# Kernel optimization log

Measured on AMD Instinct MI355X. Metric: run time of the kernel, lower is better.

## Reference

```python
import jax, jax.numpy as jnp
import numpy as np

N, E, G = 150000, 300000, 4096   # nodes, edges, graphs
H, L = 256, 7                    # hidden_channels, num_gc_layers
ATOM_FEATS, ATOM_VOCAB = 9, 64
BOND_FEATS, BOND_VOCAB = 3, 8
BN_EPS = 1e-5
MSG_EPS = 1e-7


def setup_inputs() -> dict:
    key = jax.random.key(0)
    ks = jax.random.split(key, 10)
    return dict(
        x=jax.random.randint(ks[0], (N, ATOM_FEATS), 0, ATOM_VOCAB),
        edge_index=jax.random.randint(ks[1], (2, E), 0, N),
        edge_attr=jax.random.randint(ks[2], (E, BOND_FEATS), 0, BOND_VOCAB),
        batch=jnp.sort(jax.random.randint(ks[3], (N,), 0, G)),
        atom_emb=jax.random.normal(ks[4], (ATOM_FEATS, ATOM_VOCAB, H), jnp.float32) * 0.02,
        bond_emb=jax.random.normal(ks[5], (BOND_FEATS, BOND_VOCAB, H), jnp.float32) * 0.02,
        vn_weight=jnp.zeros((1, H), jnp.float32),  # Embedding(1,H) init to 0
        conv_w=jax.random.normal(ks[6], (L, H, H), jnp.float32) / np.float32(np.sqrt(H)),
        conv_b=jnp.zeros((L, H), jnp.float32),
        norm_gamma=jnp.ones((L, H), jnp.float32),
        norm_beta=jnp.zeros((L, H), jnp.float32),
        vn_w=jax.random.normal(ks[7], (L - 1, 2, H, H), jnp.float32) / np.float32(np.sqrt(H)),
        vn_b=jnp.zeros((L - 1, 2, H), jnp.float32),
        vn_gamma=jnp.ones((L - 1, 2, H), jnp.float32),
        vn_beta=jnp.zeros((L - 1, 2, H), jnp.float32),
    )


def _bn(x, gamma, beta):
    # BatchNorm1d in training mode (biased batch stats over the node axis)
    mu = jnp.mean(x, axis=0)
    var = jnp.mean(jnp.square(x - mu), axis=0)
    return (x - mu) * jax.lax.rsqrt(var + BN_EPS) * gamma + beta


def _genconv(h, src, dst, edge_emb, w, b):
    # GENConv, aggr='add', mlp_layers=1: msg = relu(x_j + e) + eps; out = Linear(x + sum_agg)
    msg = jax.nn.relu(h[src] + edge_emb) + MSG_EPS            # [E,H]
    agg = jax.ops.segment_sum(msg, dst, num_segments=N)       # [N,H]
    return (h + agg) @ w + b


def reference(x, edge_index, edge_attr, batch, atom_emb, bond_emb, vn_weight,
              conv_w, conv_b, norm_gamma, norm_beta, vn_w, vn_b, vn_gamma, vn_beta):
    src, dst = edge_index[0], edge_index[1]
    # AtomEncoder: sum of per-feature embeddings
    h = jnp.take(atom_emb[0], x[:, 0], axis=0)
    for f in range(1, ATOM_FEATS):
        h = h + jnp.take(atom_emb[f], x[:, f], axis=0)
    # virtual node embedding (one per graph, gathered init from Embedding(1,H))
    vn = jnp.broadcast_to(vn_weight[0], (G, H))
    h = h + vn[batch]
    # BondEncoder (conv_encode_edge=False -> encode once)
    edge_emb = jnp.take(bond_emb[0], edge_attr[:, 0], axis=0)
    for f in range(1, BOND_FEATS):
        edge_emb = edge_emb + jnp.take(bond_emb[f], edge_attr[:, f], axis=0)
    # res+ block: GENConv -> [BN -> ReLU -> VN update -> GENConv -> +res]*
    h = _genconv(h, src, dst, edge_emb, conv_w[0], conv_b[0])
    for layer in range(1, L):
        h2 = jax.nn.relu(_bn(h, norm_gamma[layer - 1], norm_beta[layer - 1]))
        # virtual node: pool + residual, 2-layer MLP (Linear->BN->ReLU twice)
        vn_t = jax.ops.segment_sum(h2, batch, num_segments=G) + vn
        for j in range(2):
            vn_t = jax.nn.relu(_bn(vn_t @ vn_w[layer - 1, j] + vn_b[layer - 1, j],
                                   vn_gamma[layer - 1, j], vn_beta[layer - 1, j]))
        vn = vn_t
        h2 = h2 + vn[batch]
        h = _genconv(h2, src, dst, edge_emb, conv_w[layer], conv_b[layer]) + h
    h = _bn(h, norm_gamma[L - 1], norm_beta[L - 1])
    return jax.ops.segment_sum(h, batch, num_segments=G)  # global_add_pool -> [G,H]
```

## Files before the change

### kernel.cpp

```cpp
#include <hip/hip_runtime.h>
#include <hip/hip_bf16.h>


#define Ncnt 150000
#define Ecnt 300000
#define Gcnt 4096
#define Hc 256
#define Lcnt 7
#define BN_EPS 1e-5f
#define MSG_EPS 1e-7f

typedef __hip_bfloat16 bf16;
typedef __attribute__((ext_vector_type(8))) short bf16x8;
typedef __attribute__((ext_vector_type(8))) unsigned short u16x8;
typedef __attribute__((ext_vector_type(4))) float f32x4;

static __device__ __forceinline__ int imin(int a, int b) { return a < b ? a : b; }

static __device__ __forceinline__ float bs2f(unsigned short s) {
  unsigned u = ((unsigned)s) << 16;
  union { unsigned u; float f; } c; c.u = u; return c.f;
}
static __device__ __forceinline__ unsigned short f2bs(float f) {
  bf16 h = __float2bfloat16(f);
  union { bf16 h; unsigned short s; } c; c.h = h; return c.s;
}
static __device__ __forceinline__ float4 bf4tof4(ushort4 u) {
  float4 r; r.x = bs2f(u.x); r.y = bs2f(u.y); r.z = bs2f(u.z); r.w = bs2f(u.w); return r;
}
static __device__ __forceinline__ ushort4 f4tobf4(float4 v) {
  ushort4 u; u.x = f2bs(v.x); u.y = f2bs(v.y); u.z = f2bs(v.z); u.w = f2bs(v.w); return u;
}

static __device__ __forceinline__ void gll16(const bf16* g, const short* l) {
  __builtin_amdgcn_global_load_lds((const __attribute__((address_space(1))) void*)g,
                                   (__attribute__((address_space(3))) void*)l, 16, 0, 0);
}

__global__ __launch_bounds__(256) void k_zero(float* __restrict__ p, int n) {
  int i = blockIdx.x * 256 + threadIdx.x;
  if (i < n) p[i] = 0.f;
}
__global__ __launch_bounds__(256) void k_zero_int(int* __restrict__ p, int n) {
  int i = blockIdx.x * 256 + threadIdx.x;
  if (i < n) p[i] = 0;
}
__global__ void k_diag(float* __restrict__ out, float v) { out[0] = v; }

__global__ __launch_bounds__(256) void k_bnprep(float* __restrict__ stats,
                                                const float* __restrict__ gamma, const float* __restrict__ beta,
                                                float* __restrict__ scb, float* __restrict__ bbb, float invM) {
  int c = threadIdx.x;
  float mu = stats[c] * invM;
  float var = stats[Hc + c] * invM - mu * mu;
  float sc = rsqrtf(var + BN_EPS) * gamma[c];
  scb[c] = sc;
  bbb[c] = beta[c] - mu * sc;
  stats[c] = 0.f;
  stats[Hc + c] = 0.f;
}

__global__ __launch_bounds__(256) void k_count(const int* __restrict__ ei, int* __restrict__ cnt) {
  int e = blockIdx.x * 256 + threadIdx.x;
  if (e < Ecnt) atomicAdd(&cnt[ei[Ecnt + e]], 1);
}
__global__ __launch_bounds__(256) void k_scan1(const int* __restrict__ cnt, int* __restrict__ rowptr,
                                               int* __restrict__ bsum, int n) {
  __shared__ int sh[256];
  int t = threadIdx.x;
  int i = blockIdx.x * 256 + t;
  int v = (i < n) ? cnt[i] : 0;
  sh[t] = v;
  __syncthreads();
#pragma unroll
  for (int off = 1; off < 256; off <<= 1) {
    int u = (t >= off) ? sh[t - off] : 0;
    __syncthreads();
    sh[t] += u;
    __syncthreads();
  }
  if (i < n) rowptr[i] = sh[t] - v;
  if (t == 255) bsum[blockIdx.x] = sh[255];
}
__global__ __launch_bounds__(1024) void k_scan2(int* __restrict__ bsum, int nb) {
  __shared__ int sh[1024];
  int t = threadIdx.x;
  int v = (t < nb) ? bsum[t] : 0;
  sh[t] = v;
  __syncthreads();
#pragma unroll
  for (int off = 1; off < 1024; off <<= 1) {
    int u = (t >= off) ? sh[t - off] : 0;
    __syncthreads();
    sh[t] += u;
    __syncthreads();
  }
  if (t < nb) bsum[t] = sh[t] - v;
}
__global__ __launch_bounds__(256) void k_scan3(int* __restrict__ rowptr, int* __restrict__ cursor,
                                               const int* __restrict__ bsum, int n) {
  int i = blockIdx.x * 256 + threadIdx.x;
  if (i < n) {
    int v = rowptr[i] + bsum[blockIdx.x];
    rowptr[i] = v;
    cursor[i] = v;
  }
  if (i == 0) rowptr[n] = Ecnt;
}
__global__ __launch_bounds__(256) void k_scatter(const int* __restrict__ ei, const int* __restrict__ ea,
                                                 const int* __restrict__ batch, int* __restrict__ cursor,
                                                 int2* __restrict__ erec) {
  int e = blockIdx.x * 256 + threadIdx.x;
  if (e < Ecnt) {
    int d = ei[Ecnt + e];
    int s = ei[e];
    int packed = ea[e * 3] | (ea[e * 3 + 1] << 3) | (ea[e * 3 + 2] << 6) | (batch[s] << 9);
    int pos = atomicAdd(&cursor[d], 1);
    erec[pos] = make_int2(s, packed);
  }
}

__global__ __launch_bounds__(256) void k_prep_w(const float* __restrict__ W, bf16* __restrict__ hi,
                                                bf16* __restrict__ lo, int nmats) {
  int c = blockIdx.x * 256 + threadIdx.x;
  if (c >= nmats * 8192) return;
  int lane = c & 63;
  int t = c >> 6;
  int kc8 = t & 7;
  int nt = (t >> 3) & 15;
  int m = t >> 7;
  int n = nt * 16 + (lane & 15);
  int k0 = kc8 * 32 + (lane >> 4) * 8;
  bf16x8 hv, lv;
#pragma unroll
  for (int j = 0; j < 8; ++j) {
    float w = W[(size_t)m * 65536 + (size_t)(k0 + j) * 256 + n];
    unsigned short h = f2bs(w);
    float res = w - bs2f(h);
    hv[j] = (short)h;
    lv[j] = (short)f2bs(res);
  }
  *(bf16x8*)&hi[(size_t)c * 8] = hv;
  *(bf16x8*)&lo[(size_t)c * 8] = lv;
}

__global__ __launch_bounds__(256) void k_atom_encode(const int* __restrict__ x,
                                                     const float* __restrict__ aemb,
                                                     const float* __restrict__ vnw,
                                                     bf16* __restrict__ P) {
  int wave = threadIdx.x >> 6, lane = threadIdx.x & 63;
  int r = blockIdx.x * 4 + wave;
  if (r >= Ncnt) return;
  int c4 = lane * 4;
  const int* xr = x + (size_t)r * 9;
  float4 v = *(const float4*)&vnw[c4];
#pragma unroll
  for (int f = 0; f < 9; ++f) {
    float4 e = *(const float4*)&aemb[(size_t)((f << 6) + xr[f]) * Hc + c4];
    v.x += e.x; v.y += e.y; v.z += e.z; v.w += e.w;
  }
  *(ushort4*)&P[(size_t)r * Hc + c4] = f4tobf4(v);
}

__global__ __launch_bounds__(256) void k_init_vn(float* __restrict__ vn, float* __restrict__ vnt,
                                                 const float* __restrict__ vnw) {
  int idx = blockIdx.x * 256 + threadIdx.x;
  float v = vnw[idx & (Hc - 1)];
  vn[idx] = v;
  vnt[idx] = v;
}

__global__ __launch_bounds__(256) void k_agg(const bf16* __restrict__ P, bf16* __restrict__ T,
                                             const int* __restrict__ rowptr, const int2* __restrict__ erec,
                                             const float* __restrict__ bemb,
                                             const float* __restrict__ vn, const int* __restrict__ batch,
                                             const float* __restrict__ scb, const float* __restrict__ bbb) {
  int hw = threadIdx.x >> 5, lane = threadIdx.x & 31;
  int r = blockIdx.x * 8 + hw;
  if (r >= Ncnt) return;
  int c8 = lane * 8;
  bool hasbn = (scb != nullptr);
  float sc[8], bb[8];
  if (hasbn) {
    float4 s0 = *(const float4*)&scb[c8], s1 = *(const float4*)&scb[c8 + 4];
    float4 b0 = *(const float4*)&bbb[c8], b1 = *(const float4*)&bbb[c8 + 4];
    sc[0] = s0.x; sc[1] = s0.y; sc[2] = s0.z; sc[3] = s0.w;
    sc[4] = s1.x; sc[5] = s1.y; sc[6] = s1.z; sc[7] = s1.w;
    bb[0] = b0.x; bb[1] = b0.y; bb[2] = b0.z; bb[3] = b0.w;
    bb[4] = b1.x; bb[5] = b1.y; bb[6] = b1.z; bb[7] = b1.w;
  }
  float acc[8];
  {
    u16x8 pv = *(const u16x8*)&P[(size_t)r * Hc + c8];
    if (hasbn) {
      const float* vr = &vn[(size_t)batch[r] * Hc + c8];
      float4 w0 = *(const float4*)vr, w1 = *(const float4*)(vr + 4);
      float w[8] = {w0.x, w0.y, w0.z, w0.w, w1.x, w1.y, w1.z, w1.w};
#pragma unroll
      for (int k = 0; k < 8; ++k) acc[k] = fmaxf(fmaf(bs2f(pv[k]), sc[k], bb[k]), 0.f) + w[k];
    } else {
#pragma unroll
      for (int k = 0; k < 8; ++k) acc[k] = bs2f(pv[k]);
    }
  }
  int j0 = rowptr[r], j1 = rowptr[r + 1];
  if (j0 < j1) {
    int2 er = erec[j0];
    for (int j = j0; j < j1; ++j) {
      int2 ern = (j + 1 < j1) ? erec[j + 1] : er;
      int s = er.x;
      int a0 = er.y & 7, a1 = (er.y >> 3) & 7, a2 = (er.y >> 6) & 7, g = er.y >> 9;
      u16x8 sv = *(const u16x8*)&P[(size_t)s * Hc + c8];
      const float* e0 = &bemb[(size_t)a0 * Hc + c8];
      const float* e1 = &bemb[(size_t)(8 + a1) * Hc + c8];
      const float* e2 = &bemb[(size_t)(16 + a2) * Hc + c8];
      float4 e0a = *(const float4*)e0, e0b = *(const float4*)(e0 + 4);
      float4 e1a = *(const float4*)e1, e1b = *(const float4*)(e1 + 4);
      float4 e2a = *(const float4*)e2, e2b = *(const float4*)(e2 + 4);
      float em[8] = {e0a.x + e1a.x + e2a.x, e0a.y + e1a.y + e2a.y,
                     e0a.z + e1a.z + e2a.z, e0a.w + e1a.w + e2a.w,
                     e0b.x + e1b.x + e2b.x, e0b.y + e1b.y + e2b.y,
                     e0b.z + e1b.z + e2b.z, e0b.w + e1b.w + e2b.w};
      if (hasbn) {
        const float* vr = &vn[(size_t)g * Hc + c8];
        float4 w0 = *(const float4*)vr, w1 = *(const float4*)(vr + 4);
        float w[8] = {w0.x, w0.y, w0.z, w0.w, w1.x, w1.y, w1.z, w1.w};
#pragma unroll
        for (int k = 0; k < 8; ++k) {
          float v = fmaxf(fmaf(bs2f(sv[k]), sc[k], bb[k]), 0.f) + w[k];
          acc[k] += fmaxf(v + em[k], 0.f) + MSG_EPS;
        }
      } else {
#pragma unroll
        for (int k = 0; k < 8; ++k)
          acc[k] += fmaxf(bs2f(sv[k]) + em[k], 0.f) + MSG_EPS;
      }
      er = ern;
    }
  }
  u16x8 ov;
#pragma unroll
  for (int k = 0; k < 8; ++k) ov[k] = f2bs(acc[k]);
  *(u16x8*)&T[(size_t)r * Hc + c8] = ov;
}

__global__ __launch_bounds__(256) void k_seg_vn(const bf16* __restrict__ P, const int* __restrict__ batch,
                                                float* __restrict__ vnt,
                                                const float* __restrict__ scb, const float* __restrict__ bbb) {
  int wave = threadIdx.x >> 6, lane = threadIdx.x & 63;
  int base = (blockIdx.x * 4 + wave) * 64;
  if (base >= Ncnt) return;
  int c4 = lane * 4;
  float4 scv = *(const float4*)&scb[c4];
  float4 bbv = *(const float4*)&bbb[c4];
  int end = imin(base + 64, Ncnt);
  float4 acc = make_float4(0.f, 0.f, 0.f, 0.f);
  int curg = batch[base];
  for (int r = base; r < end; ++r) {
    int g = batch[r];
    float4 v = bf4tof4(*(const ushort4*)&P[(size_t)r * Hc + c4]);
    v.x = fmaxf(fmaf(v.x, scv.x, bbv.x), 0.f); v.y = fmaxf(fmaf(v.y, scv.y, bbv.y), 0.f);
    v.z = fmaxf(fmaf(v.z, scv.z, bbv.z), 0.f); v.w = fmaxf(fmaf(v.w, scv.w, bbv.w), 0.f);
    if (g != curg) {
      float* d = &vnt[(size_t)curg * Hc + c4];
      atomicAdd(d, acc.x); atomicAdd(d + 1, acc.y); atomicAdd(d + 2, acc.z); atomicAdd(d + 3, acc.w);
      acc = make_float4(0.f, 0.f, 0.f, 0.f);
      curg = g;
    }
    acc.x += v.x; acc.y += v.y; acc.z += v.z; acc.w += v.w;
  }
  float* d = &vnt[(size_t)curg * Hc + c4];
  atomicAdd(d, acc.x); atomicAdd(d + 1, acc.y); atomicAdd(d + 2, acc.z); atomicAdd(d + 3, acc.w);
}

__global__ __launch_bounds__(256) void k_vn_relu(const float* __restrict__ in, float* __restrict__ out,
                                                 float* __restrict__ out2,
                                                 const float* __restrict__ stats,
                                                 const float* __restrict__ gamma, const float* __restrict__ beta,
                                                 float invM) {
  int idx = blockIdx.x * 256 + threadIdx.x;
  int c = idx & (Hc - 1);
  float mu = stats[c] * invM;
  float var = stats[Hc + c] * invM - mu * mu;
  float sc = rsqrtf(var + BN_EPS) * gamma[c];
  float bb = beta[c] - mu * sc;
  float v = fmaxf(fmaf(in[idx], sc, bb), 0.f);
  out[idx] = v;
  out2[idx] = v;
}

__global__ __launch_bounds__(256) void k_bn_pool(const bf16* __restrict__ P, const int* __restrict__ batch,
                                                 float* __restrict__ out,
                                                 const float* __restrict__ scb, const float* __restrict__ bbb) {
  int wave = threadIdx.x >> 6, lane = threadIdx.x & 63;
  int base = (blockIdx.x * 4 + wave) * 64;
  if (base >= Ncnt) return;
  int c4 = lane * 4;
  float4 scv = *(const float4*)&scb[c4];
  float4 bbv = *(const float4*)&bbb[c4];
  int end = imin(base + 64, Ncnt);
  float4 acc = make_float4(0.f, 0.f, 0.f, 0.f);
  int curg = batch[base];
  for (int r = base; r < end; ++r) {
    int g = batch[r];
    float4 v = bf4tof4(*(const ushort4*)&P[(size_t)r * Hc + c4]);
    v.x = fmaf(v.x, scv.x, bbv.x); v.y = fmaf(v.y, scv.y, bbv.y);
    v.z = fmaf(v.z, scv.z, bbv.z); v.w = fmaf(v.w, scv.w, bbv.w);
    if (g != curg) {
      float* d = &out[(size_t)curg * Hc + c4];
      atomicAdd(d, acc.x); atomicAdd(d + 1, acc.y); atomicAdd(d + 2, acc.z); atomicAdd(d + 3, acc.w);
      acc = make_float4(0.f, 0.f, 0.f, 0.f);
      curg = g;
    }
    acc.x += v.x; acc.y += v.y; acc.z += v.z; acc.w += v.w;
  }
  float* d = &out[(size_t)curg * Hc + c4];
  atomicAdd(d, acc.x); atomicAdd(d + 1, acc.y); atomicAdd(d + 2, acc.z); atomicAdd(d + 3, acc.w);
}

__global__ __launch_bounds__(256, 3) void k_gemm_mfma(const bf16* __restrict__ A, const bf16* __restrict__ Whi,
                                                      const bf16* __restrict__ Wlo, const float* __restrict__ bias,
                                                      const bf16* __restrict__ R, bf16* __restrict__ C,
                                                      float* __restrict__ stats, int M) {
  __shared__ __attribute__((aligned(16))) short As[64 * 64];
  __shared__ __attribute__((aligned(16))) unsigned short Cs[16 * 264];
  __shared__ float lsum[256], lsq[256];
  int tid = threadIdx.x;
  int wave = tid >> 6, lane = tid & 63;
  int quad = lane >> 4, l15 = lane & 15;
  int wc = wave * 64;
  int row0 = blockIdx.x * 64;

  lsum[tid] = 0.f;
  lsq[tid] = 0.f;

  int sr[2], sjg[2];
#pragma unroll
  for (int i = 0; i < 2; ++i) {
    int s = i * 256 + tid;
    sr[i] = s >> 3;
    sjg[i] = (s & 7) ^ (sr[i] & 7);
  }

  f32x4 acc[4][4];
#pragma unroll
  for (int i = 0; i < 4; ++i)
#pragma unroll
    for (int j = 0; j < 4; ++j) acc[i][j] = (f32x4){0.f, 0.f, 0.f, 0.f};

  for (int kci = 0; kci < 4; ++kci) {
    int kc = kci * 64;
#pragma unroll
    for (int i = 0; i < 2; ++i) {
      int ar = row0 + sr[i]; if (ar >= M) ar = M - 1;
      gll16(A + (size_t)ar * Hc + kc + sjg[i] * 8, &As[(i * 256 + wave * 64) * 8]);
    }
    __syncthreads();
#pragma unroll
    for (int ks = 0; ks < 2; ++ks) {
      int kc8 = kci * 2 + ks;
      int g = ks * 4 + quad;
      bf16x8 af[4];
#pragma unroll
      for (int mi = 0; mi < 4; ++mi) {
        int row = mi * 16 + l15;
        af[mi] = *(const bf16x8*)&As[row * 64 + (g ^ (row & 7)) * 8];
      }
#pragma unroll
      for (int nii = 0; nii < 4; ++nii) {
        int nt = wave * 4 + nii;
        size_t fo = (((size_t)nt * 8 + kc8) * 64 + lane) * 8;
        bf16x8 bh = *(const bf16x8*)&Whi[fo];
        bf16x8 bl = *(const bf16x8*)&Wlo[fo];
#pragma unroll
        for (int mi = 0; mi < 4; ++mi) {
          acc[mi][nii] = __builtin_amdgcn_mfma_f32_16x16x32_bf16(af[mi], bh, acc[mi][nii], 0, 0, 0);
          acc[mi][nii] = __builtin_amdgcn_mfma_f32_16x16x32_bf16(af[mi], bl, acc[mi][nii], 0, 0, 0);
        }
      }
    }
    __syncthreads();
  }

  float s8[8], q8[8];
#pragma unroll
  for (int k = 0; k < 8; ++k) { s8[k] = 0.f; q8[k] = 0.f; }
  int cg8 = (tid & 31) * 8;

  for (int p = 0; p < 4; ++p) {
    int lr0 = quad * 4;
#pragma unroll
    for (int ni = 0; ni < 4; ++ni) {
      int col = wc + ni * 16 + l15;
      float bcol = bias[col];
#pragma unroll
      for (int j = 0; j < 4; ++j)
        Cs[(lr0 + j) * 264 + col] = f2bs(acc[p][ni][j] + bcol);
    }
    __syncthreads();
#pragma unroll
    for (int i = 0; i < 2; ++i) {
      int slot = i * 256 + tid;
      int lr = slot >> 5;
      int grow = row0 + p * 16 + lr;
      if (grow < M) {
        u16x8 cv = *(const u16x8*)&Cs[lr * 264 + cg8];
        float v[8];
#pragma unroll
        for (int k = 0; k < 8; ++k) v[k] = bs2f(cv[k]);
        if (R) {
          u16x8 rv = *(const u16x8*)&R[(size_t)grow * Hc + cg8];
#pragma unroll
          for (int k = 0; k < 8; ++k) v[k] += bs2f(rv[k]);
        }
        u16x8 ov;
#pragma unroll
        for (int k = 0; k < 8; ++k) {
          ov[k] = f2bs(v[k]);
          s8[k] += v[k];
          q8[k] = fmaf(v[k], v[k], q8[k]);
        }
        *(u16x8*)&C[(size_t)grow * Hc + cg8] = ov;
      }
    }
    __syncthreads();
  }

#pragma unroll
  for (int k = 0; k < 8; ++k) {
    atomicAdd(&lsum[cg8 + k], s8[k]);
    atomicAdd(&lsq[cg8 + k], q8[k]);
  }
  __syncthreads();
  atomicAdd(&stats[tid], lsum[tid]);
  atomicAdd(&stats[Hc + tid], lsq[tid]);
}

__global__ __launch_bounds__(256) void k_gemm_f32(const float* __restrict__ A, const float* __restrict__ W,
                                                  const float* __restrict__ bias, float* __restrict__ C,
                                                  float* __restrict__ statsOut,
                                                  const float* __restrict__ statsIn,
                                                  const float* __restrict__ gIn, const float* __restrict__ bIn,
                                                  float invM, int M) {
  __shared__ float As[64][68];
  __shared__ float Ws[64][68];
  __shared__ float lsum[64], lsq[64];
  int tid = threadIdx.x;
  int row0 = blockIdx.x * 64;
  int col0 = blockIdx.y * 64;
  int tx = tid & 15, ty = tid >> 4;
  if (tid < 64) { lsum[tid] = 0.f; lsq[tid] = 0.f; }
  float acc[4][4] = {{0.f}};
  for (int k0 = 0; k0 < 256; k0 += 64) {
#pragma unroll
    for (int i = 0; i < 4; ++i) {
      int lin = tid + i * 256;
      int r = lin >> 4;
      int c4 = (lin & 15) << 2;
      int gr = row0 + r;
      float4 v = make_float4(0.f, 0.f, 0.f, 0.f);
      if (gr < M) v = *(const float4*)&A[(size_t)gr * Hc + k0 + c4];
      if (statsIn) {
        float4 sv = *(const float4*)&statsIn[k0 + c4];
        float4 qv = *(const float4*)&statsIn[Hc + k0 + c4];
        float4 gv = *(const float4*)&gIn[k0 + c4];
        float4 bv = *(const float4*)&bIn[k0 + c4];
        float mu, var, sc, bb;
        mu = sv.x * invM; var = qv.x * invM - mu * mu; sc = rsqrtf(var + BN_EPS) * gv.x; bb = bv.x - mu * sc;
        v.x = fmaxf(fmaf(v.x, sc, bb), 0.f);
        mu = sv.y * invM; var = qv.y * invM - mu * mu; sc = rsqrtf(var + BN_EPS) * gv.y; bb = bv.y - mu * sc;
        v.y = fmaxf(fmaf(v.y, sc, bb), 0.f);
        mu = sv.z * invM; var = qv.z * invM - mu * mu; sc = rsqrtf(var + BN_EPS) * gv.z; bb = bv.z - mu * sc;
        v.z = fmaxf(fmaf(v.z, sc, bb), 0.f);
        mu = sv.w * invM; var = qv.w * invM - mu * mu; sc = rsqrtf(var + BN_EPS) * gv.w; bb = bv.w - mu * sc;
        v.w = fmaxf(fmaf(v.w, sc, bb), 0.f);
      }
      As[r][c4] = v.x; As[r][c4 + 1] = v.y; As[r][c4 + 2] = v.z; As[r][c4 + 3] = v.w;
      float4 w = *(const float4*)&W[(size_t)(k0 + r) * Hc + col0 + c4];
      Ws[r][c4] = w.x; Ws[r][c4 + 1] = w.y; Ws[r][c4 + 2] = w.z; Ws[r][c4 + 3] = w.w;
    }
    __syncthreads();
#pragma unroll
    for (int k = 0; k < 64; ++k) {
      float a[4], w[4];
#pragma unroll
      for (int i = 0; i < 4; ++i) a[i] = As[ty * 4 + i][k];
#pragma unroll
      for (int j = 0; j < 4; ++j) w[j] = Ws[k][tx * 4 + j];
#pragma unroll
      for (int i = 0; i < 4; ++i)
#pragma unroll
        for (int j = 0; j < 4; ++j) acc[i][j] = fmaf(a[i], w[j], acc[i][j]);
    }
    __syncthreads();
  }
  float cs[4] = {0.f, 0.f, 0.f, 0.f}, cq[4] = {0.f, 0.f, 0.f, 0.f};
#pragma unroll
  for (int i = 0; i < 4; ++i) {
    int gr = row0 + ty * 4 + i;
    if (gr >= M) break;
#pragma unroll
    for (int j = 0; j < 4; ++j) {
      int gc = col0 + tx * 4 + j;
      float v = acc[i][j] + bias[gc];
      C[(size_t)gr * Hc + gc] = v;
      cs[j] += v;
      cq[j] = fmaf(v, v, cq[j]);
    }
  }
#pragma unroll
  for (int j = 0; j < 4; ++j) {
    atomicAdd(&lsum[tx * 4 + j], cs[j]);
    atomicAdd(&lsq[tx * 4 + j], cq[j]);
  }
  __syncthreads();
  if (tid < 64) {
    atomicAdd(&statsOut[col0 + tid], lsum[tid]);
    atomicAdd(&statsOut[Hc + col0 + tid], lsq[tid]);
  }
}

extern "C" void kernel_launch(void* const* d_in, const int* in_sizes, int n_in,
                              void* d_out, int out_size, void* d_ws, size_t ws_size,
                              hipStream_t stream) {
  const int* x = (const int*)d_in[0];
  const int* ei = (const int*)d_in[1];
  const int* ea = (const int*)d_in[2];
  const int* batch = (const int*)d_in[3];
  const float* aemb = (const float*)d_in[4];
  const float* bemb = (const float*)d_in[5];
  const float* vnw = (const float*)d_in[6];
  const float* conv_w = (const float*)d_in[7];
  const float* conv_b = (const float*)d_in[8];
  const float* ngamma = (const float*)d_in[9];
  const float* nbeta = (const float*)d_in[10];
  const float* vn_w = (const float*)d_in[11];
  const float* vn_b = (const float*)d_in[12];
  const float* vn_g = (const float*)d_in[13];
  const float* vn_be = (const float*)d_in[14];
  float* out = (float*)d_out;

  const size_t NODE = (size_t)Ncnt * Hc;
  const size_t GH = (size_t)Gcnt * Hc;
  const int nScanBlk = (Ncnt + 255) / 256;

  size_t off = 0;
  char* base = (char*)d_ws;
  auto take = [&](size_t bytes) { size_t o = off; off += (bytes + 15) & ~(size_t)15; return o; };
  float* vn = (float*)(base + take(GH * 4));
  float* vnt = (float*)(base + take(GH * 4));
  float* vnu = (float*)(base + take(GH * 4));
  float* vnv = (float*)(base + take(GH * 4));
  float* statsN = (float*)(base + take(2 * Hc * 4));
  float* statsV1 = (float*)(base + take(2 * Hc * 4));
  float* statsV2 = (float*)(base + take(2 * Hc * 4));
  float* scbN = (float*)(base + take(Hc * 4));
  float* bbbN = (float*)(base + take(Hc * 4));
  int* rowptr = (int*)(base + take((size_t)(Ncnt + 1) * 4));
  int* cursor = (int*)(base + take((size_t)Ncnt * 4));
  int2* erec = (int2*)(base + take((size_t)Ecnt * 8));
  int* bsum = (int*)(base + take((size_t)nScanBlk * 4));
  bf16* P = (bf16*)(base + take(NODE * 2));
  bf16* T = (bf16*)(base + take(NODE * 2));
  bf16* WhiC = (bf16*)(base + take((size_t)Lcnt * 65536 * 2));
  bf16* WloC = (bf16*)(base + take((size_t)Lcnt * 65536 * 2));
  const size_t NEED = off;
  if (ws_size < NEED) {
    k_zero<<<(int)((GH + 255) / 256), 256, 0, stream>>>(out, (int)GH);
    k_diag<<<1, 1, 0, stream>>>(out, 100000.f + (float)(ws_size / (1024.0 * 1024.0)));
    return;
  }

  const int eBlk = (Ecnt + 255) / 256;
  const int nWaveBlk = (Ncnt + 3) / 4;
  const int aggBlk = (Ncnt + 7) / 8;
  const int segBlk = (Ncnt + 255) / 256;
  const int ggN = (Ncnt + 63) / 64;
  const dim3 gv(Gcnt / 64, 4);
  const float invN = 1.f / Ncnt;
  const float invG = 1.f / Gcnt;

  k_zero_int<<<nScanBlk, 256, 0, stream>>>(cursor, Ncnt);
  k_count<<<eBlk, 256, 0, stream>>>(ei, cursor);
  k_scan1<<<nScanBlk, 256, 0, stream>>>(cursor, rowptr, bsum, Ncnt);
  k_scan2<<<1, 1024, 0, stream>>>(bsum, nScanBlk);
  k_scan3<<<nScanBlk, 256, 0, stream>>>(rowptr, cursor, bsum, Ncnt);
  k_scatter<<<eBlk, 256, 0, stream>>>(ei, ea, batch, cursor, erec);

  k_prep_w<<<(Lcnt * 8192 + 255) / 256, 256, 0, stream>>>(conv_w, WhiC, WloC, Lcnt);

  k_atom_encode<<<nWaveBlk, 256, 0, stream>>>(x, aemb, vnw, P);
  k_init_vn<<<(int)(GH / 256), 256, 0, stream>>>(vn, vnt, vnw);
  k_agg<<<aggBlk, 256, 0, stream>>>(P, T, rowptr, erec, bemb, nullptr, nullptr, nullptr, nullptr);
  k_zero<<<2, 256, 0, stream>>>(statsN, 2 * Hc);
  k_gemm_mfma<<<ggN, 256, 0, stream>>>(T, WhiC, WloC, conv_b, nullptr, P, statsN, Ncnt);

  for (int l = 1; l < Lcnt; ++l) {
    int p = l - 1;
    k_bnprep<<<1, 256, 0, stream>>>(statsN, ngamma + (size_t)p * Hc, nbeta + (size_t)p * Hc,
                                    scbN, bbbN, invN);
    k_seg_vn<<<segBlk, 256, 0, stream>>>(P, batch, vnt, scbN, bbbN);
    k_zero<<<4, 256, 0, stream>>>(statsV1, 4 * Hc);
    k_gemm_f32<<<gv, 256, 0, stream>>>(vnt, vn_w + (size_t)(2 * p) * 65536,
                                       vn_b + (size_t)(2 * p) * Hc, vnu, statsV1,
                                       nullptr, nullptr, nullptr, invG, Gcnt);
    k_gemm_f32<<<gv, 256, 0, stream>>>(vnu, vn_w + (size_t)(2 * p + 1) * 65536,
                                       vn_b + (size_t)(2 * p + 1) * Hc, vnv, statsV2,
                                       statsV1, vn_g + (size_t)(2 * p) * Hc,
                                       vn_be + (size_t)(2 * p) * Hc, invG, Gcnt);
    k_vn_relu<<<(int)(GH / 256), 256, 0, stream>>>(vnv, vn, vnt, statsV2,
                                                   vn_g + (size_t)(2 * p + 1) * Hc,
                                                   vn_be + (size_t)(2 * p + 1) * Hc, invG);
    k_agg<<<aggBlk, 256, 0, stream>>>(P, T, rowptr, erec, bemb, vn, batch, scbN, bbbN);
    k_gemm_mfma<<<ggN, 256, 0, stream>>>(T, WhiC + (size_t)l * 65536, WloC + (size_t)l * 65536,
                                         conv_b + (size_t)l * Hc, P, P, statsN, Ncnt);
  }

  k_bnprep<<<1, 256, 0, stream>>>(statsN, ngamma + (size_t)(Lcnt - 1) * Hc,
                                  nbeta + (size_t)(Lcnt - 1) * Hc, scbN, bbbN, invN);
  k_zero<<<(int)((GH + 255) / 256), 256, 0, stream>>>(out, (int)GH);
  k_bn_pool<<<segBlk, 256, 0, stream>>>(P, batch, out, scbN, bbbN);
}
```

Measured before the change: 2.285 ms.

## Fuse edge aggregation into MFMA GEMM kernel with ping-pong node buffers

Merges the per-node edge aggregation into the GEMM kernel. Each block gathers messages for its 64 rows directly into a full-K swizzled LDS tile, then runs the MFMA matmul, BN stats and residual epilogue. This removes the intermediate T buffer's global write and re-read and one launch per layer. Two node buffers are swapped each layer so neighbour reads don't race with outputs. The cost is a larger LDS footprint (64x256 tile), which may lower occupancy and gather latency hiding.

```diff
diff --git a/kernel.cpp b/kernel.cpp
--- a/kernel.cpp
+++ b/kernel.cpp
@@ -30,11 +30,6 @@
 }
 static __device__ __forceinline__ ushort4 f4tobf4(float4 v) {
   ushort4 u; u.x = f2bs(v.x); u.y = f2bs(v.y); u.z = f2bs(v.z); u.w = f2bs(v.w); return u;
-}
-
-static __device__ __forceinline__ void gll16(const bf16* g, const short* l) {
-  __builtin_amdgcn_global_load_lds((const __attribute__((address_space(1))) void*)g,
-                                   (__attribute__((address_space(3))) void*)l, 16, 0, 0);
 }
 
 __global__ __launch_bounds__(256) void k_zero(float* __restrict__ p, int n) {
@@ -168,80 +163,6 @@
   float v = vnw[idx & (Hc - 1)];
   vn[idx] = v;
   vnt[idx] = v;
-}
-
-__global__ __launch_bounds__(256) void k_agg(const bf16* __restrict__ P, bf16* __restrict__ T,
-                                             const int* __restrict__ rowptr, const int2* __restrict__ erec,
-                                             const float* __restrict__ bemb,
-                                             const float* __restrict__ vn, const int* __restrict__ batch,
-                                             const float* __restrict__ scb, const float* __restrict__ bbb) {
-  int hw = threadIdx.x >> 5, lane = threadIdx.x & 31;
-  int r = blockIdx.x * 8 + hw;
-  if (r >= Ncnt) return;
-  int c8 = lane * 8;
-  bool hasbn = (scb != nullptr);
-  float sc[8], bb[8];
-  if (hasbn) {
-    float4 s0 = *(const float4*)&scb[c8], s1 = *(const float4*)&scb[c8 + 4];
-    float4 b0 = *(const float4*)&bbb[c8], b1 = *(const float4*)&bbb[c8 + 4];
-    sc[0] = s0.x; sc[1] = s0.y; sc[2] = s0.z; sc[3] = s0.w;
-    sc[4] = s1.x; sc[5] = s1.y; sc[6] = s1.z; sc[7] = s1.w;
-    bb[0] = b0.x; bb[1] = b0.y; bb[2] = b0.z; bb[3] = b0.w;
-    bb[4] = b1.x; bb[5] = b1.y; bb[6] = b1.z; bb[7] = b1.w;
-  }
-  float acc[8];
-  {
-    u16x8 pv = *(const u16x8*)&P[(size_t)r * Hc + c8];
-    if (hasbn) {
-      const float* vr = &vn[(size_t)batch[r] * Hc + c8];
-      float4 w0 = *(const float4*)vr, w1 = *(const float4*)(vr + 4);
-      float w[8] = {w0.x, w0.y, w0.z, w0.w, w1.x, w1.y, w1.z, w1.w};
-#pragma unroll
-      for (int k = 0; k < 8; ++k) acc[k] = fmaxf(fmaf(bs2f(pv[k]), sc[k], bb[k]), 0.f) + w[k];
-    } else {
-#pragma unroll
-      for (int k = 0; k < 8; ++k) acc[k] = bs2f(pv[k]);
-    }
-  }
-  int j0 = rowptr[r], j1 = rowptr[r + 1];
-  if (j0 < j1) {
-    int2 er = erec[j0];
-    for (int j = j0; j < j1; ++j) {
-      int2 ern = (j + 1 < j1) ? erec[j + 1] : er;
-      int s = er.x;
-      int a0 = er.y & 7, a1 = (er.y >> 3) & 7, a2 = (er.y >> 6) & 7, g = er.y >> 9;
-      u16x8 sv = *(const u16x8*)&P[(size_t)s * Hc + c8];
-      const float* e0 = &bemb[(size_t)a0 * Hc + c8];
-      const float* e1 = &bemb[(size_t)(8 + a1) * Hc + c8];
-      const float* e2 = &bemb[(size_t)(16 + a2) * Hc + c8];
-      float4 e0a = *(const float4*)e0, e0b = *(const float4*)(e0 + 4);
-      float4 e1a = *(const float4*)e1, e1b = *(const float4*)(e1 + 4);
-      float4 e2a = *(const float4*)e2, e2b = *(const float4*)(e2 + 4);
-      float em[8] = {e0a.x + e1a.x + e2a.x, e0a.y + e1a.y + e2a.y,
-                     e0a.z + e1a.z + e2a.z, e0a.w + e1a.w + e2a.w,
-                     e0b.x + e1b.x + e2b.x, e0b.y + e1b.y + e2b.y,
-                     e0b.z + e1b.z + e2b.z, e0b.w + e1b.w + e2b.w};
-      if (hasbn) {
-        const float* vr = &vn[(size_t)g * Hc + c8];
-        float4 w0 = *(const float4*)vr, w1 = *(const float4*)(vr + 4);
-        float w[8] = {w0.x, w0.y, w0.z, w0.w, w1.x, w1.y, w1.z, w1.w};
-#pragma unroll
-        for (int k = 0; k < 8; ++k) {
-          float v = fmaxf(fmaf(bs2f(sv[k]), sc[k], bb[k]), 0.f) + w[k];
-          acc[k] += fmaxf(v + em[k], 0.f) + MSG_EPS;
-        }
-      } else {
-#pragma unroll
-        for (int k = 0; k < 8; ++k)
-          acc[k] += fmaxf(bs2f(sv[k]) + em[k], 0.f) + MSG_EPS;
-      }
-      er = ern;
-    }
-  }
-  u16x8 ov;
-#pragma unroll
-  for (int k = 0; k < 8; ++k) ov[k] = f2bs(acc[k]);
-  *(u16x8*)&T[(size_t)r * Hc + c8] = ov;
 }
 
 __global__ __launch_bounds__(256) void k_seg_vn(const bf16* __restrict__ P, const int* __restrict__ batch,
@@ -318,74 +239,136 @@
   atomicAdd(d, acc.x); atomicAdd(d + 1, acc.y); atomicAdd(d + 2, acc.z); atomicAdd(d + 3, acc.w);
 }
 
-__global__ __launch_bounds__(256, 3) void k_gemm_mfma(const bf16* __restrict__ A, const bf16* __restrict__ Whi,
-                                                      const bf16* __restrict__ Wlo, const float* __restrict__ bias,
-                                                      const bf16* __restrict__ R, bf16* __restrict__ C,
-                                                      float* __restrict__ stats, int M) {
-  __shared__ __attribute__((aligned(16))) short As[64 * 64];
+__global__ __launch_bounds__(256, 3) void k_agg_gemm(const bf16* __restrict__ P,
+                                                     const int* __restrict__ rowptr, const int2* __restrict__ erec,
+                                                     const float* __restrict__ bemb,
+                                                     const float* __restrict__ vn, const int* __restrict__ batch,
+                                                     const float* __restrict__ scb, const float* __restrict__ bbb,
+                                                     const bf16* __restrict__ Whi, const bf16* __restrict__ Wlo,
+                                                     const float* __restrict__ bias,
+                                                     const bf16* __restrict__ R, bf16* __restrict__ C,
+                                                     float* __restrict__ stats, int M) {
+  __shared__ __attribute__((aligned(16))) unsigned short As[64 * 256];
   __shared__ __attribute__((aligned(16))) unsigned short Cs[16 * 264];
   __shared__ float lsum[256], lsq[256];
   int tid = threadIdx.x;
   int wave = tid >> 6, lane = tid & 63;
   int quad = lane >> 4, l15 = lane & 15;
-  int wc = wave * 64;
+  int hw = tid >> 5, hl = tid & 31;
+  int c8 = hl * 8;
   int row0 = blockIdx.x * 64;
 
   lsum[tid] = 0.f;
   lsq[tid] = 0.f;
 
-  int sr[2], sjg[2];
-#pragma unroll
-  for (int i = 0; i < 2; ++i) {
-    int s = i * 256 + tid;
-    sr[i] = s >> 3;
-    sjg[i] = (s & 7) ^ (sr[i] & 7);
-  }
-
-  f32x4 acc[4][4];
-#pragma unroll
-  for (int i = 0; i < 4; ++i)
-#pragma unroll
-    for (int j = 0; j < 4; ++j) acc[i][j] = (f32x4){0.f, 0.f, 0.f, 0.f};
-
-  for (int kci = 0; kci < 4; ++kci) {
-    int kc = kci * 64;
-#pragma unroll
-    for (int i = 0; i < 2; ++i) {
-      int ar = row0 + sr[i]; if (ar >= M) ar = M - 1;
-      gll16(A + (size_t)ar * Hc + kc + sjg[i] * 8, &As[(i * 256 + wave * 64) * 8]);
-    }
-    __syncthreads();
-#pragma unroll
-    for (int ks = 0; ks < 2; ++ks) {
-      int kc8 = kci * 2 + ks;
-      int g = ks * 4 + quad;
-      bf16x8 af[4];
-#pragma unroll
-      for (int mi = 0; mi < 4; ++mi) {
-        int row = mi * 16 + l15;
-        af[mi] = *(const bf16x8*)&As[row * 64 + (g ^ (row & 7)) * 8];
+  bool hasbn = (scb != nullptr);
+  float sc[8], bb[8];
+  if (hasbn) {
+    float4 s0 = *(const float4*)&scb[c8], s1 = *(const float4*)&scb[c8 + 4];
+    float4 b0 = *(const float4*)&bbb[c8], b1 = *(const float4*)&bbb[c8 + 4];
+    sc[0] = s0.x; sc[1] = s0.y; sc[2] = s0.z; sc[3] = s0.w;
+    sc[4] = s1.x; sc[5] = s1.y; sc[6] = s1.z; sc[7] = s1.w;
+    bb[0] = b0.x; bb[1] = b0.y; bb[2] = b0.z; bb[3] = b0.w;
+    bb[4] = b1.x; bb[5] = b1.y; bb[6] = b1.z; bb[7] = b1.w;
+  }
+  int kci = c8 >> 6;
+  int jg = (c8 >> 3) & 7;
+  for (int q = 0; q < 8; ++q) {
+    int rl = hw * 8 + q;
+    int r = row0 + rl;
+    float acc[8];
+    if (r < M) {
+      u16x8 pv = *(const u16x8*)&P[(size_t)r * Hc + c8];
+      if (hasbn) {
+        const float* vr = &vn[(size_t)batch[r] * Hc + c8];
+        float4 w0 = *(const float4*)vr, w1 = *(const float4*)(vr + 4);
+        float w[8] = {w0.x, w0.y, w0.z, w0.w, w1.x, w1.y, w1.z, w1.w};
+#pragma unroll
+        for (int k = 0; k < 8; ++k) acc[k] = fmaxf(fmaf(bs2f(pv[k]), sc[k], bb[k]), 0.f) + w[k];
+      } else {
+#pragma unroll
+        for (int k = 0; k < 8; ++k) acc[k] = bs2f(pv[k]);
       }
-#pragma unroll
-      for (int nii = 0; nii < 4; ++nii) {
-        int nt = wave * 4 + nii;
-        size_t fo = (((size_t)nt * 8 + kc8) * 64 + lane) * 8;
-        bf16x8 bh = *(const bf16x8*)&Whi[fo];
-        bf16x8 bl = *(const bf16x8*)&Wlo[fo];
-#pragma unroll
-        for (int mi = 0; mi < 4; ++mi) {
-          acc[mi][nii] = __builtin_amdgcn_mfma_f32_16x16x32_bf16(af[mi], bh, acc[mi][nii], 0, 0, 0);
-          acc[mi][nii] = __builtin_amdgcn_mfma_f32_16x16x32_bf16(af[mi], bl, acc[mi][nii], 0, 0, 0);
+      int j0 = rowptr[r], j1 = rowptr[r + 1];
+      if (j0 < j1) {
+        int2 er = erec[j0];
+        for (int j = j0; j < j1; ++j) {
+          int2 ern = (j + 1 < j1) ? erec[j + 1] : er;
+          int s = er.x;
+          int a0 = er.y & 7, a1 = (er.y >> 3) & 7, a2 = (er.y >> 6) & 7, g = er.y >> 9;
+          u16x8 sv = *(const u16x8*)&P[(size_t)s * Hc + c8];
+          const float* e0 = &bemb[(size_t)a0 * Hc + c8];
+          const float* e1 = &bemb[(size_t)(8 + a1) * Hc + c8];
+          const float* e2 = &bemb[(size_t)(16 + a2) * Hc + c8];
+          float4 e0a = *(const float4*)e0, e0b = *(const float4*)(e0 + 4);
+          float4 e1a = *(const float4*)e1, e1b = *(const float4*)(e1 + 4);
+          float4 e2a = *(const float4*)e2, e2b = *(const float4*)(e2 + 4);
+          float em[8] = {e0a.x + e1a.x + e2a.x, e0a.y + e1a.y + e2a.y,
+                         e0a.z + e1a.z + e2a.z, e0a.w + e1a.w + e2a.w,
+                         e0b.x + e1b.x + e2b.x, e0b.y + e1b.y + e2b.y,
+                         e0b.z + e1b.z + e2b.z, e0b.w + e1b.w + e2b.w};
+          if (hasbn) {
+            const float* vr = &vn[(size_t)g * Hc + c8];
+            float4 w0 = *(const float4*)vr, w1 = *(const float4*)(vr + 4);
+            float w[8] = {w0.x, w0.y, w0.z, w0.w, w1.x, w1.y, w1.z, w1.w};
+#pragma unroll
+            for (int k = 0; k < 8; ++k) {
+              float v = fmaxf(fmaf(bs2f(sv[k]), sc[k], bb[k]), 0.f) + w[k];
+              acc[k] += fmaxf(v + em[k], 0.f) + MSG_EPS;
+            }
+          } else {
+#pragma unroll
+            for (int k = 0; k < 8; ++k)
+              acc[k] += fmaxf(bs2f(sv[k]) + em[k], 0.f) + MSG_EPS;
+          }
+          er = ern;
         }
       }
-    }
-    __syncthreads();
+    } else {
+#pragma unroll
+      for (int k = 0; k < 8; ++k) acc[k] = 0.f;
+    }
+    u16x8 ov;
+#pragma unroll
+    for (int k = 0; k < 8; ++k) ov[k] = f2bs(acc[k]);
+    *(u16x8*)&As[rl * 256 + kci * 64 + ((jg ^ (rl & 7)) << 3)] = ov;
+  }
+  __syncthreads();
+
+  int wc = wave * 64;
+  f32x4 acc4[4][4];
+#pragma unroll
+  for (int i = 0; i < 4; ++i)
+#pragma unroll
+    for (int j = 0; j < 4; ++j) acc4[i][j] = (f32x4){0.f, 0.f, 0.f, 0.f};
+
+#pragma unroll
+  for (int kc8 = 0; kc8 < 8; ++kc8) {
+    int kcs = kc8 >> 1;
+    int g = (kc8 & 1) * 4 + quad;
+    bf16x8 af[4];
+#pragma unroll
+    for (int mi = 0; mi < 4; ++mi) {
+      int row = mi * 16 + l15;
+      af[mi] = *(const bf16x8*)&As[row * 256 + kcs * 64 + ((g ^ (row & 7)) << 3)];
+    }
+#pragma unroll
+    for (int nii = 0; nii < 4; ++nii) {
+      int nt = wave * 4 + nii;
+      size_t fo = (((size_t)nt * 8 + kc8) * 64 + lane) * 8;
+      bf16x8 bh = *(const bf16x8*)&Whi[fo];
+      bf16x8 bl = *(const bf16x8*)&Wlo[fo];
+#pragma unroll
+      for (int mi = 0; mi < 4; ++mi) {
+        acc4[mi][nii] = __builtin_amdgcn_mfma_f32_16x16x32_bf16(af[mi], bh, acc4[mi][nii], 0, 0, 0);
+        acc4[mi][nii] = __builtin_amdgcn_mfma_f32_16x16x32_bf16(af[mi], bl, acc4[mi][nii], 0, 0, 0);
+      }
+    }
   }
 
   float s8[8], q8[8];
 #pragma unroll
   for (int k = 0; k < 8; ++k) { s8[k] = 0.f; q8[k] = 0.f; }
-  int cg8 = (tid & 31) * 8;
 
   for (int p = 0; p < 4; ++p) {
     int lr0 = quad * 4;
@@ -395,7 +378,7 @@
       float bcol = bias[col];
 #pragma unroll
       for (int j = 0; j < 4; ++j)
-        Cs[(lr0 + j) * 264 + col] = f2bs(acc[p][ni][j] + bcol);
+        Cs[(lr0 + j) * 264 + col] = f2bs(acc4[p][ni][j] + bcol);
     }
     __syncthreads();
 #pragma unroll
@@ -404,12 +387,12 @@
       int lr = slot >> 5;
       int grow = row0 + p * 16 + lr;
       if (grow < M) {
-        u16x8 cv = *(const u16x8*)&Cs[lr * 264 + cg8];
+        u16x8 cv = *(const u16x8*)&Cs[lr * 264 + c8];
         float v[8];
 #pragma unroll
         for (int k = 0; k < 8; ++k) v[k] = bs2f(cv[k]);
         if (R) {
-          u16x8 rv = *(const u16x8*)&R[(size_t)grow * Hc + cg8];
+          u16x8 rv = *(const u16x8*)&R[(size_t)grow * Hc + c8];
 #pragma unroll
           for (int k = 0; k < 8; ++k) v[k] += bs2f(rv[k]);
         }
@@ -420,7 +403,7 @@
           s8[k] += v[k];
           q8[k] = fmaf(v[k], v[k], q8[k]);
         }
-        *(u16x8*)&C[(size_t)grow * Hc + cg8] = ov;
+        *(u16x8*)&C[(size_t)grow * Hc + c8] = ov;
       }
     }
     __syncthreads();
@@ -428,8 +411,8 @@
 
 #pragma unroll
   for (int k = 0; k < 8; ++k) {
-    atomicAdd(&lsum[cg8 + k], s8[k]);
-    atomicAdd(&lsq[cg8 + k], q8[k]);
+    atomicAdd(&lsum[c8 + k], s8[k]);
+    atomicAdd(&lsq[c8 + k], q8[k]);
   }
   __syncthreads();
   atomicAdd(&stats[tid], lsum[tid]);
@@ -560,8 +543,8 @@
   int* cursor = (int*)(base + take((size_t)Ncnt * 4));
   int2* erec = (int2*)(base + take((size_t)Ecnt * 8));
   int* bsum = (int*)(base + take((size_t)nScanBlk * 4));
-  bf16* P = (bf16*)(base + take(NODE * 2));
-  bf16* T = (bf16*)(base + take(NODE * 2));
+  bf16* P0 = (bf16*)(base + take(NODE * 2));
+  bf16* P1 = (bf16*)(base + take(NODE * 2));
   bf16* WhiC = (bf16*)(base + take((size_t)Lcnt * 65536 * 2));
   bf16* WloC = (bf16*)(base + take((size_t)Lcnt * 65536 * 2));
   const size_t NEED = off;
@@ -573,7 +556,6 @@
 
   const int eBlk = (Ecnt + 255) / 256;
   const int nWaveBlk = (Ncnt + 3) / 4;
-  const int aggBlk = (Ncnt + 7) / 8;
   const int segBlk = (Ncnt + 255) / 256;
   const int ggN = (Ncnt + 63) / 64;
   const dim3 gv(Gcnt / 64, 4);
@@ -589,17 +571,21 @@
 
   k_prep_w<<<(Lcnt * 8192 + 255) / 256, 256, 0, stream>>>(conv_w, WhiC, WloC, Lcnt);
 
-  k_atom_encode<<<nWaveBlk, 256, 0, stream>>>(x, aemb, vnw, P);
+  k_atom_encode<<<nWaveBlk, 256, 0, stream>>>(x, aemb, vnw, P0);
   k_init_vn<<<(int)(GH / 256), 256, 0, stream>>>(vn, vnt, vnw);
-  k_agg<<<aggBlk, 256, 0, stream>>>(P, T, rowptr, erec, bemb, nullptr, nullptr, nullptr, nullptr);
   k_zero<<<2, 256, 0, stream>>>(statsN, 2 * Hc);
-  k_gemm_mfma<<<ggN, 256, 0, stream>>>(T, WhiC, WloC, conv_b, nullptr, P, statsN, Ncnt);
+  bf16* pa = P0;
+  bf16* pb = P1;
+  k_agg_gemm<<<ggN, 256, 0, stream>>>(pa, rowptr, erec, bemb,
+                                      nullptr, nullptr, nullptr, nullptr,
+                                      WhiC, WloC, conv_b, nullptr, pb, statsN, Ncnt);
+  { bf16* t = pa; pa = pb; pb = t; }
 
   for (int l = 1; l < Lcnt; ++l) {
     int p = l - 1;
     k_bnprep<<<1, 256, 0, stream>>>(statsN, ngamma + (size_t)p * Hc, nbeta + (size_t)p * Hc,
                                     scbN, bbbN, invN);
-    k_seg_vn<<<segBlk, 256, 0, stream>>>(P, batch, vnt, scbN, bbbN);
+    k_seg_vn<<<segBlk, 256, 0, stream>>>(pa, batch, vnt, scbN, bbbN);
     k_zero<<<4, 256, 0, stream>>>(statsV1, 4 * Hc);
     k_gemm_f32<<<gv, 256, 0, stream>>>(vnt, vn_w + (size_t)(2 * p) * 65536,
                                        vn_b + (size_t)(2 * p) * Hc, vnu, statsV1,
@@ -611,13 +597,15 @@
     k_vn_relu<<<(int)(GH / 256), 256, 0, stream>>>(vnv, vn, vnt, statsV2,
                                                    vn_g + (size_t)(2 * p + 1) * Hc,
                                                    vn_be + (size_t)(2 * p + 1) * Hc, invG);
-    k_agg<<<aggBlk, 256, 0, stream>>>(P, T, rowptr, erec, bemb, vn, batch, scbN, bbbN);
-    k_gemm_mfma<<<ggN, 256, 0, stream>>>(T, WhiC + (size_t)l * 65536, WloC + (size_t)l * 65536,
-                                         conv_b + (size_t)l * Hc, P, P, statsN, Ncnt);
+    k_agg_gemm<<<ggN, 256, 0, stream>>>(pa, rowptr, erec, bemb,
+                                        vn, batch, scbN, bbbN,
+                                        WhiC + (size_t)l * 65536, WloC + (size_t)l * 65536,
+                                        conv_b + (size_t)l * Hc, pa, pb, statsN, Ncnt);
+    { bf16* t = pa; pa = pb; pb = t; }
   }
 
   k_bnprep<<<1, 256, 0, stream>>>(statsN, ngamma + (size_t)(Lcnt - 1) * Hc,
                                   nbeta + (size_t)(Lcnt - 1) * Hc, scbN, bbbN, invN);
   k_zero<<<(int)((GH + 255) / 256), 256, 0, stream>>>(out, (int)GH);
-  k_bn_pool<<<segBlk, 256, 0, stream>>>(P, batch, out, scbN, bbbN);
-}
+  k_bn_pool<<<segBlk, 256, 0, stream>>>(pa, batch, out, scbN, bbbN);
+}
```

Result: slower. 2.361 ms (+3.4%).
